# Performance work log

Hardware: AMD Instinct MI355X
Metric: run time of the kernel (lower is better)

## Reference

```python
import jax, jax.numpy as jnp
import numpy as np

H = 97
IN = 9
N_NODES = 100000
N_EDGES = 800000
N_GRAPHS = 4096
N_LAYERS = 7
N_STEPS = 7
BN_EPS = 1e-5


def setup_inputs() -> dict:
    key = jax.random.key(0)
    ks = iter(jax.random.split(key, 40))
    sc = 0.1  # param init scale
    inp = {}
    inp['x'] = jax.random.normal(next(ks), (N_NODES, IN), jnp.float32)
    inp['edge_index'] = jax.random.randint(next(ks), (2, N_EDGES), 0, N_NODES, jnp.int32)
    inp['batch'] = jnp.sort(jax.random.randint(next(ks), (N_NODES,), 0, N_GRAPHS, jnp.int32))
    inp['num_graphs'] = N_GRAPHS
    inp['lin1_W'] = jax.random.normal(next(ks), (IN, H), jnp.float32) * sc
    inp['lin1_b'] = jax.random.normal(next(ks), (H,), jnp.float32) * sc
    for nm in ['Wk', 'Wq', 'Wv', 'Ws']:
        inp['conv_' + nm] = jax.random.normal(next(ks), (N_LAYERS, H, H), jnp.float32) * sc
    for nm in ['bk', 'bq', 'bv', 'bs']:
        inp['conv_' + nm] = jax.random.normal(next(ks), (N_LAYERS, H), jnp.float32) * sc
    inp['gru_Wih'] = jax.random.normal(next(ks), (N_LAYERS, H, 3 * H), jnp.float32) * sc
    inp['gru_Whh'] = jax.random.normal(next(ks), (N_LAYERS, H, 3 * H), jnp.float32) * sc
    inp['gru_bih'] = jax.random.normal(next(ks), (N_LAYERS, 3 * H), jnp.float32) * sc
    inp['gru_bhh'] = jax.random.normal(next(ks), (N_LAYERS, 3 * H), jnp.float32) * sc
    inp['bn_gamma'] = jnp.ones((N_LAYERS - 1, H), jnp.float32)
    inp['bn_beta'] = jnp.zeros((N_LAYERS - 1, H), jnp.float32)
    inp['bn_mean'] = jnp.zeros((N_LAYERS - 1, H), jnp.float32)
    inp['bn_var'] = jnp.ones((N_LAYERS - 1, H), jnp.float32)
    inp['gat_W'] = jax.random.normal(next(ks), (H, H), jnp.float32) * sc
    inp['gat_asrc'] = jax.random.normal(next(ks), (H,), jnp.float32) * sc
    inp['gat_adst'] = jax.random.normal(next(ks), (H,), jnp.float32) * sc
    inp['gat_b'] = jax.random.normal(next(ks), (H,), jnp.float32) * sc
    inp['molgru_Wih'] = jax.random.normal(next(ks), (H, 3 * H), jnp.float32) * sc
    inp['molgru_Whh'] = jax.random.normal(next(ks), (H, 3 * H), jnp.float32) * sc
    inp['molgru_bih'] = jax.random.normal(next(ks), (3 * H,), jnp.float32) * sc
    inp['molgru_bhh'] = jax.random.normal(next(ks), (3 * H,), jnp.float32) * sc
    inp['lin2_W'] = jax.random.normal(next(ks), (H, 1), jnp.float32) * sc
    inp['lin2_b'] = jax.random.normal(next(ks), (1,), jnp.float32) * sc
    return inp


def _gru(xin, h, Wih, Whh, bih, bhh):
    gi = xin @ Wih + bih  # [N, 3H]
    gh = h @ Whh + bhh
    ir, iz, inn = jnp.split(gi, 3, axis=-1)
    hr, hz, hn = jnp.split(gh, 3, axis=-1)
    r = jax.nn.sigmoid(ir + hr)
    z = jax.nn.sigmoid(iz + hz)
    n = jnp.tanh(inn + r * hn)
    return (1.0 - z) * n + z * h


def _resgated(x, src, dst, Wk, bk, Wq, bq, Wv, bv, Ws, bs, n_nodes):
    # PyG ResGatedGraphConv: out_i = Ws x_i + sum_j sigmoid(Wk x_i + Wq x_j) * (Wv x_j)
    k = x @ Wk + bk
    q = x @ Wq + bq
    v = x @ Wv + bv
    msg = jax.nn.sigmoid(k[dst] + q[src]) * v[src]  # [E, H]
    agg = jax.ops.segment_sum(msg, dst, num_segments=n_nodes)
    return agg + (x @ Ws + bs)


def _forward(x, lin1_W, lin1_b, conv_Wk, conv_bk, conv_Wq, conv_bq, conv_Wv, conv_bv,
             conv_Ws, conv_bs, gru_Wih, gru_Whh, gru_bih, gru_bhh,
             bn_gamma, bn_beta, bn_mean, bn_var,
             gat_W, gat_asrc, gat_adst, gat_b,
             molgru_Wih, molgru_Whh, molgru_bih, molgru_bhh,
             lin2_W, lin2_b, edge_index, batch, num_graphs):
    src, dst = edge_index[0], edge_index[1]
    n_nodes = x.shape[0]
    x = jax.nn.leaky_relu(x @ lin1_W + lin1_b, 0.01)
    # layer 0 (gate_conv + gru)
    h = jax.nn.elu(_resgated(x, src, dst, conv_Wk[0], conv_bk[0], conv_Wq[0], conv_bq[0],
                             conv_Wv[0], conv_bv[0], conv_Ws[0], conv_bs[0], n_nodes))
    x = jax.nn.relu(_gru(h, x, gru_Wih[0], gru_Whh[0], gru_bih[0], gru_bhh[0]))
    # layers 1..6 with eval-mode BatchNorm (dropout inactive in eval)
    for l in range(1, N_LAYERS):
        h = jax.nn.elu(_resgated(x, src, dst, conv_Wk[l], conv_bk[l], conv_Wq[l], conv_bq[l],
                                 conv_Wv[l], conv_bv[l], conv_Ws[l], conv_bs[l], n_nodes))
        b = l - 1
        h = (h - bn_mean[b]) * (bn_gamma[b] / jnp.sqrt(bn_var[b] + BN_EPS)) + bn_beta[b]
        x = jax.nn.relu(_gru(h, x, gru_Wih[l], gru_Whh[l], gru_bih[l], gru_bhh[l]))
    # molecule readout: global_add_pool then bipartite GAT (heads=1) over node->graph edges
    out = jax.nn.relu(jax.ops.segment_sum(x, batch, num_segments=num_graphs))  # [G, H]
    xs = x @ gat_W          # source projections, fixed over timesteps
    a_s = xs @ gat_asrc     # [N]
    for _ in range(N_STEPS):
        a_d = (out @ gat_W) @ gat_adst  # [G]
        alpha = jax.nn.leaky_relu(a_s + a_d[batch], 0.01)  # one score per node-edge
        m = jax.ops.segment_max(alpha, batch, num_segments=num_graphs)
        m = jnp.where(jnp.isfinite(m), m, 0.0)
        e = jnp.exp(alpha - m[batch])
        s = jax.ops.segment_sum(e, batch, num_segments=num_graphs)
        w = e / s[batch]  # segment softmax over each graph's nodes
        hg = jax.ops.segment_sum(w[:, None] * xs, batch, num_segments=num_graphs) + gat_b
        h = jax.nn.elu(hg)
        out = jax.nn.relu(_gru(h, out, molgru_Wih, molgru_Whh, molgru_bih, molgru_bhh))
    return out @ lin2_W + lin2_b  # [G, 1]


def reference(x, edge_index, batch, num_graphs, lin1_W, lin1_b, conv_Wk, conv_bk, conv_Wq,
              conv_bq, conv_Wv, conv_bv, conv_Ws, conv_bs, gru_Wih, gru_Whh, gru_bih, gru_bhh,
              bn_gamma, bn_beta, bn_mean, bn_var, gat_W, gat_asrc, gat_adst, gat_b,
              molgru_Wih, molgru_Whh, molgru_bih, molgru_bhh, lin2_W, lin2_b):
    return _forward(x, lin1_W, lin1_b, conv_Wk, conv_bk, conv_Wq, conv_bq, conv_Wv, conv_bv,
                    conv_Ws, conv_bs, gru_Wih, gru_Whh, gru_bih, gru_bhh,
                    bn_gamma, bn_beta, bn_mean, bn_var,
                    gat_W, gat_asrc, gat_adst, gat_b,
                    molgru_Wih, molgru_Whh, molgru_bih, molgru_bhh,
                    lin2_W, lin2_b, edge_index, batch, num_graphs)
```

## Files before the change

kernel.cpp:

```cpp
#include <hip/hip_runtime.h>

#define NN 100000
#define NNP 100032
#define NE 800000
#define NG 4096
#define HH 97
#define HP 128
#define NB 391

#define WGF_SET_STRIDE 147456
#define WCF_LAYER_STRIDE 98304

typedef unsigned short u16;
typedef unsigned int u32;
typedef __attribute__((ext_vector_type(8))) short short8v;
typedef __attribute__((ext_vector_type(4))) float f32x4;

__device__ __forceinline__ float sigm_(float x){ return 1.f/(1.f+__expf(-x)); }
__device__ __forceinline__ float lrelu01_(float x){ return x>0.f? x : 0.01f*x; }
__device__ __forceinline__ float tanh_(float t){ float e2=__expf(2.f*t); return 1.f-2.f/(e2+1.f); }
__device__ __forceinline__ float b2f(u16 u){ union{u32 i; float f;} t; t.i=(u32)u<<16; return t.f; }
__device__ __forceinline__ u16 f2b(float x){ union{float f; u32 i;} t; t.f=x; u32 r=t.i+0x7FFFu+((t.i>>16)&1u); return (u16)(r>>16); }

__device__ __forceinline__ void store_bf16x4(u16* p, float v0, float v1, float v2, float v3){
  ushort4 s; s.x = f2b(v0); s.y = f2b(v1); s.z = f2b(v2); s.w = f2b(v3);
  *(ushort4*)p = s;
}

__device__ __forceinline__ f32x4 mfma16(short8v a, short8v b, f32x4 c){
  return __builtin_amdgcn_mfma_f32_16x16x32_bf16(a, b, c, 0, 0, 0);
}

__global__ void k_pack_convw(const float* __restrict__ Wk, const float* __restrict__ Wq,
                             const float* __restrict__ Wv, const float* __restrict__ Ws,
                             u16* __restrict__ out){
  int idx = blockIdx.x*256 + threadIdx.x;
  if (idx >= 7*4*8*3*2*512) return;
  int e = idx & 7, lane = (idx>>3) & 63;
  int r = idx >> 9;
  int term = r & 1; r >>= 1;
  int ks = r % 3; r /= 3;
  int t = r & 7; r >>= 3;
  int w = r & 3; int l = r >> 2;
  int k = ks*32 + (lane>>4)*8 + e;
  int n = (w*8 + t)*16 + (lane & 15);
  int m = n>>7, h = n & 127;
  float val = 0.f;
  if (k < HH && h < HH){
    const float* W = (m==0)? Wk : (m==1)? Wq : (m==2)? Wv : Ws;
    val = W[l*9409 + k*97 + h];
  }
  u16 hi = f2b(val);
  out[idx] = (term==0)? hi : f2b(val - b2f(hi));
}

__global__ void k_pack_gruw(const float* __restrict__ gih, const float* __restrict__ ghh,
                            const float* __restrict__ mih, const float* __restrict__ mhh,
                            u16* __restrict__ out){
  int idx = blockIdx.x*256 + threadIdx.x;
  if (idx >= 8*8*3*3*4*512) return;
  int e = idx & 7, lane = (idx>>3) & 63;
  int r = idx >> 9;
  int mat = r & 3; r >>= 2;
  int ks = r % 3; r /= 3;
  int j = r % 3; r /= 3;
  int bt = r & 7; int set = r >> 3;
  int k = ks*32 + (lane>>4)*8 + e;
  int n = (j*8 + bt)*16 + (lane & 15);
  int jg = n>>7, g = n & 127;
  float val = 0.f;
  if (k < HH && g < HH){
    const float* srcp;
    if (mat < 2) srcp = (set < 7)? gih + (size_t)set*28227 : mih;
    else         srcp = (set < 7)? ghh + (size_t)set*28227 : mhh;
    val = srcp[k*291 + jg*97 + g];
  }
  u16 hi = f2b(val);
  out[idx] = ((mat & 1)==0)? hi : f2b(val - b2f(hi));
}

__global__ void k_pack_gatw(const float* __restrict__ gatW, u16* __restrict__ out){
  int idx = blockIdx.x*256 + threadIdx.x;
  if (idx >= 2*4*8*512) return;
  int e = idx & 7, lane = (idx>>3) & 63, t = (idx>>9) & 7;
  int ks = (idx>>12) & 3, term = idx>>14;
  int k = ks*32 + (lane>>4)*8 + e;
  int h = t*16 + (lane & 15);
  float val = (k < HH && h < HH)? gatW[k*97 + h] : 0.f;
  u16 hi = f2b(val);
  out[idx] = (term==0)? hi : f2b(val - b2f(hi));
}

__global__ void k_pack_w96(const float* __restrict__ Wk, const float* __restrict__ Wq,
                           const float* __restrict__ Wv, const float* __restrict__ Ws,
                           const float* __restrict__ gih, const float* __restrict__ ghh,
                           const float* __restrict__ mih, const float* __restrict__ mhh,
                           float* __restrict__ out){
  int idx = blockIdx.x*256 + threadIdx.x;
  if (idx < 7*512){
    int l = idx >> 9, c = idx & 511;
    int m = c >> 7, h = c & 127;
    float v = 0.f;
    if (h < HH){
      const float* W = (m==0)? Wk : (m==1)? Wq : (m==2)? Wv : Ws;
      v = W[l*9409 + 96*97 + h];
    }
    out[idx] = v;
  } else if (idx < 7*512 + 8*384){
    int r = idx - 7*512;
    int set = r / 384, n = r % 384;
    int j = n >> 7, g = n & 127;
    float v = 0.f;
    if (g < HH){
      const float* srcp = (set < 7)? gih + (size_t)set*28227 : mih;
      v = srcp[96*291 + j*97 + g];
    }
    out[idx] = v;
  } else if (idx < 7*512 + 16*384){
    int r = idx - 7*512 - 8*384;
    int set = r / 384, n = r % 384;
    int j = n >> 7, g = n & 127;
    float v = 0.f;
    if (g < HH){
      const float* srcp = (set < 7)? ghh + (size_t)set*28227 : mhh;
      v = srcp[96*291 + j*97 + g];
    }
    out[idx] = v;
  }
}

__global__ void k_pack_convb(const float* __restrict__ bk, const float* __restrict__ bq,
                             const float* __restrict__ bv, const float* __restrict__ bs,
                             float* __restrict__ out){
  int idx = blockIdx.x*256 + threadIdx.x;
  if (idx >= 7*512) return;
  int l = idx >> 9, c = idx & 511;
  int m = c >> 7, h = c & 127;
  float v = 0.f;
  if (h < HH){
    const float* B = (m==0)? bk : (m==1)? bq : (m==2)? bv : bs;
    v = B[l*97 + h];
  }
  out[idx] = v;
}

__global__ void k_pack_grub(const float* __restrict__ gbi, const float* __restrict__ gbh,
                            const float* __restrict__ mbi, const float* __restrict__ mbh,
                            float* __restrict__ obi, float* __restrict__ obh){
  int idx = blockIdx.x*256 + threadIdx.x;
  if (idx >= 8*384) return;
  int set = idx / 384, n = idx % 384;
  int j = n>>7, g = n & 127;
  float vi = 0.f, vh = 0.f;
  if (g < HH){
    const float* si = (set < 7)? gbi + set*291 : mbi;
    const float* sh = (set < 7)? gbh + set*291 : mbh;
    vi = si[j*97 + g];
    vh = sh[j*97 + g];
  }
  obi[idx] = vi; obh[idx] = vh;
}

__global__ void k_pack_misc(const float* __restrict__ gatW, const float* __restrict__ asrc,
                            const float* __restrict__ adst, const float* __restrict__ gatb,
                            const float* __restrict__ l2W, float* __restrict__ out){
  int idx = blockIdx.x*256 + threadIdx.x;
  if (idx < 16384){
    int k = idx >> 7, h = idx & 127;
    out[idx] = (k < HH && h < HH)? gatW[k*97 + h] : 0.f;
  } else if (idx < 16512){
    int h = idx - 16384; out[idx] = (h < HH)? asrc[h] : 0.f;
  } else if (idx < 16640){
    int h = idx - 16512; out[idx] = (h < HH)? adst[h] : 0.f;
  } else if (idx < 16768){
    int h = idx - 16640; out[idx] = (h < HH)? gatb[h] : 0.f;
  } else if (idx < 16896){
    int h = idx - 16768; out[idx] = (h < HH)? l2W[h] : 0.f;
  } else if (idx < 17408){
    out[idx] = 0.f;
  }
}

__global__ void k_seg(const int* __restrict__ batch, int* __restrict__ seg){
  int g = blockIdx.x*blockDim.x + threadIdx.x;
  if (g > NG) return;
  int lo = 0, hi = NN;
  while (lo < hi){ int mid = (lo+hi) >> 1; if (batch[mid] < g) lo = mid+1; else hi = mid; }
  seg[g] = lo;
}

__global__ void k_hist(const int* __restrict__ dst, int* __restrict__ cnt){
  int e = blockIdx.x*256 + threadIdx.x;
  if (e < NE) atomicAdd(&cnt[dst[e]], 1);
}

__global__ void k_scan_blk(const int* __restrict__ cnt, int* __restrict__ offs,
                           int* __restrict__ bsum){
  __shared__ int s[256];
  int b = blockIdx.x, t = threadIdx.x, i = b*256 + t;
  int v = (i < NN)? cnt[i] : 0;
  s[t] = v; __syncthreads();
  #pragma unroll
  for (int off = 1; off < 256; off <<= 1){
    int tmp = (t >= off)? s[t-off] : 0;
    __syncthreads();
    s[t] += tmp;
    __syncthreads();
  }
  if (i < NN) offs[i] = s[t] - v;
  if (t == 255) bsum[b] = s[255];
}

__global__ void k_scan_top(int* __restrict__ bsum){
  __shared__ int s[512];
  int t = threadIdx.x;
  int v = (t < NB)? bsum[t] : 0;
  s[t] = v; __syncthreads();
  #pragma unroll
  for (int off = 1; off < 512; off <<= 1){
    int tmp = (t >= off)? s[t-off] : 0;
    __syncthreads();
    s[t] += tmp;
    __syncthreads();
  }
  if (t < NB) bsum[t] = s[t] - v;
}

__global__ void k_scan_add(int* __restrict__ offs, const int* __restrict__ bsum,
                           int* __restrict__ cur){
  int b = blockIdx.x, t = threadIdx.x, i = b*256 + t;
  if (i < NN){ int o = offs[i] + bsum[b]; offs[i] = o; cur[i] = o; }
  if (i == 0) offs[NN] = NE;
}

__global__ void k_scatter(const int* __restrict__ src, const int* __restrict__ dst,
                          int* __restrict__ cur, int* __restrict__ eidx){
  int e = blockIdx.x*256 + threadIdx.x;
  if (e >= NE) return;
  int pos = atomicAdd(&cur[dst[e]], 1);
  eidx[pos] = src[e];
}

__global__ __launch_bounds__(256) void k_lin1(const float* __restrict__ x,
    const float* __restrict__ W, const float* __restrict__ b, u16* __restrict__ X0){
  int idx = blockIdx.x*256 + threadIdx.x;
  int n = idx >> 7, c = idx & 127;
  float v = 0.f;
  if (n < NN && c < HH){
    v = b[c];
    #pragma unroll
    for (int k = 0; k < 9; ++k) v += x[n*9 + k]*W[k*HH + c];
    v = lrelu01_(v);
  }
  X0[(size_t)n*HP + c] = f2b(v);
}

__global__ __launch_bounds__(256) void k_conv_mfma(const u16* __restrict__ X,
    const u16* __restrict__ WCF_l, const float* __restrict__ biasp,
    const float* __restrict__ W96C, u16* __restrict__ KQV,
    u16* __restrict__ Sh, u16* __restrict__ Sl){
  int tid = threadIdx.x;
  int w = __builtin_amdgcn_readfirstlane(tid >> 6);
  int lane = tid & 63;
  int lm = lane & 15, ls = lane >> 4;
  int m0 = blockIdx.x*64;
  f32x4 acc[4][8] = {};
  const u16* pw = WCF_l + (size_t)w*24576 + lane*8;
  for (int ks = 0; ks < 3; ++ks){
    short8v aX[4];
    #pragma unroll
    for (int rb = 0; rb < 4; ++rb)
      aX[rb] = *(const short8v*)(X + (size_t)(m0 + rb*16 + lm)*HP + ks*32 + ls*8);
    short8v wf[8][2];
    #pragma unroll
    for (int t = 0; t < 8; ++t){
      const u16* q = pw + ((t*3 + ks) << 10);
      wf[t][0] = *(const short8v*)(q);
      wf[t][1] = *(const short8v*)(q + 512);
    }
    #pragma unroll
    for (int t = 0; t < 8; ++t)
      #pragma unroll
      for (int rb = 0; rb < 4; ++rb){
        acc[rb][t] = mfma16(wf[t][0], aX[rb], acc[rb][t]);
        acc[rb][t] = mfma16(wf[t][1], aX[rb], acc[rb][t]);
      }
  }
  float x96[4];
  #pragma unroll
  for (int rb = 0; rb < 4; ++rb)
    x96[rb] = b2f(X[(size_t)(m0 + rb*16 + lm)*HP + 96]);
  #pragma unroll
  for (int t = 0; t < 8; ++t){
    int c0 = w*128 + t*16 + ls*4;
    float4 bv = *(const float4*)(biasp + c0);
    float4 w96 = *(const float4*)(W96C + c0);
    #pragma unroll
    for (int rb = 0; rb < 4; ++rb){
      int node = m0 + rb*16 + lm;
      float v0 = acc[rb][t][0] + bv.x + x96[rb]*w96.x;
      float v1 = acc[rb][t][1] + bv.y + x96[rb]*w96.y;
      float v2 = acc[rb][t][2] + bv.z + x96[rb]*w96.z;
      float v3 = acc[rb][t][3] + bv.w + x96[rb]*w96.w;
      if (w < 3){
        store_bf16x4(KQV + (size_t)node*384 + w*128 + t*16 + ls*4, v0, v1, v2, v3);
      } else {
        int co = t*16 + ls*4;
        u16 h0 = f2b(v0), h1 = f2b(v1), h2 = f2b(v2), h3 = f2b(v3);
        ushort4 hv; hv.x=h0; hv.y=h1; hv.z=h2; hv.w=h3;
        *(ushort4*)(Sh + (size_t)node*HP + co) = hv;
        store_bf16x4(Sl + (size_t)node*HP + co,
                     v0 - b2f(h0), v1 - b2f(h1), v2 - b2f(h2), v3 - b2f(h3));
      }
    }
  }
}

__global__ __launch_bounds__(256) void k_gru_mfma(const u16* __restrict__ Sh_,
    const u16* __restrict__ Sl_, const u16* __restrict__ Xin,
    const u16* __restrict__ WGF_set,
    const float* __restrict__ bihp, const float* __restrict__ bhhp,
    const float* __restrict__ W96I, const float* __restrict__ W96H,
    u16* __restrict__ Xout){
  int tid = threadIdx.x;
  int w = __builtin_amdgcn_readfirstlane(tid >> 6);
  int lane = tid & 63;
  int lm = lane & 15, ls = lane >> 4;
  int m0 = blockIdx.x*32;
  f32x4 agi[2][2][3] = {};
  f32x4 agh[2][2][3] = {};
  for (int ks = 0; ks < 3; ++ks){
    short8v aX[2], aSh[2], aSl[2];
    #pragma unroll
    for (int rb = 0; rb < 2; ++rb){
      size_t off = (size_t)(m0 + rb*16 + lm)*HP + ks*32 + ls*8;
      aX[rb]  = *(const short8v*)(Xin + off);
      aSh[rb] = *(const short8v*)(Sh_ + off);
      aSl[rb] = *(const short8v*)(Sl_ + off);
    }
    #pragma unroll
    for (int b = 0; b < 2; ++b){
      const u16* pb = WGF_set + (size_t)(2*w + b)*18432 + lane*8;
      short8v fIh[3], fIl[3], fHh[3], fHl[3];
      #pragma unroll
      for (int j = 0; j < 3; ++j){
        const u16* q = pb + ((j*3 + ks) << 11);
        fIh[j] = *(const short8v*)(q);
        fIl[j] = *(const short8v*)(q + 512);
        fHh[j] = *(const short8v*)(q + 1024);
        fHl[j] = *(const short8v*)(q + 1536);
      }
      #pragma unroll
      for (int j = 0; j < 3; ++j)
        #pragma unroll
        for (int rb = 0; rb < 2; ++rb){
          agi[rb][b][j] = mfma16(fIh[j], aSh[rb], agi[rb][b][j]);
          agi[rb][b][j] = mfma16(fIl[j], aSh[rb], agi[rb][b][j]);
          agi[rb][b][j] = mfma16(fIh[j], aSl[rb], agi[rb][b][j]);
          agh[rb][b][j] = mfma16(fHh[j], aX[rb], agh[rb][b][j]);
          agh[rb][b][j] = mfma16(fHl[j], aX[rb], agh[rb][b][j]);
        }
    }
  }
  float s96[2], x96[2];
  #pragma unroll
  for (int rb = 0; rb < 2; ++rb){
    size_t o96 = (size_t)(m0 + rb*16 + lm)*HP + 96;
    s96[rb] = b2f(Sh_[o96]) + b2f(Sl_[o96]);
    x96[rb] = b2f(Xin[o96]);
  }
  #pragma unroll
  for (int b = 0; b < 2; ++b){
    int g0 = (2*w + b)*16 + ls*4;
    float4 bi0 = *(const float4*)(bihp + g0);
    float4 bi1 = *(const float4*)(bihp + 128 + g0);
    float4 bi2 = *(const float4*)(bihp + 256 + g0);
    float4 bh0 = *(const float4*)(bhhp + g0);
    float4 bh1 = *(const float4*)(bhhp + 128 + g0);
    float4 bh2 = *(const float4*)(bhhp + 256 + g0);
    float4 wi0 = *(const float4*)(W96I + g0);
    float4 wi1 = *(const float4*)(W96I + 128 + g0);
    float4 wi2 = *(const float4*)(W96I + 256 + g0);
    float4 wh0 = *(const float4*)(W96H + g0);
    float4 wh1 = *(const float4*)(W96H + 128 + g0);
    float4 wh2 = *(const float4*)(W96H + 256 + g0);
    #pragma unroll
    for (int rb = 0; rb < 2; ++rb){
      int node = m0 + rb*16 + lm;
      ushort4 xo4 = *(const ushort4*)(Xin + (size_t)node*HP + g0);
      float xo[4] = { b2f(xo4.x), b2f(xo4.y), b2f(xo4.z), b2f(xo4.w) };
      float vout[4];
      #pragma unroll
      for (int r = 0; r < 4; ++r){
        float biv0 = ((const float*)&bi0)[r], biv1 = ((const float*)&bi1)[r], biv2 = ((const float*)&bi2)[r];
        float bhv0 = ((const float*)&bh0)[r], bhv1 = ((const float*)&bh1)[r], bhv2 = ((const float*)&bh2)[r];
        float wiv0 = ((const float*)&wi0)[r], wiv1 = ((const float*)&wi1)[r], wiv2 = ((const float*)&wi2)[r];
        float whv0 = ((const float*)&wh0)[r], whv1 = ((const float*)&wh1)[r], whv2 = ((const float*)&wh2)[r];
        float ir = agi[rb][b][0][r] + biv0 + s96[rb]*wiv0;
        float iz = agi[rb][b][1][r] + biv1 + s96[rb]*wiv1;
        float in_ = agi[rb][b][2][r] + biv2 + s96[rb]*wiv2;
        float hr = agh[rb][b][0][r] + bhv0 + x96[rb]*whv0;
        float hz = agh[rb][b][1][r] + bhv1 + x96[rb]*whv1;
        float hn = agh[rb][b][2][r] + bhv2 + x96[rb]*whv2;
        float rr = sigm_(ir + hr);
        float zz = sigm_(iz + hz);
        float nn2 = tanh_(in_ + rr*hn);
        float v = (1.f - zz)*nn2 + zz*xo[r];
        vout[r] = fmaxf(v, 0.f);
      }
      store_bf16x4(Xout + (size_t)node*HP + g0, vout[0], vout[1], vout[2], vout[3]);
    }
  }
}

__global__ __launch_bounds__(256) void k_xs_mfma(const u16* __restrict__ X,
    const u16* __restrict__ GATF, u16* __restrict__ XS){
  int tid = threadIdx.x;
  int w = tid >> 6, lane = tid & 63;
  int lm = lane & 15, ls = lane >> 4;
  int m0 = blockIdx.x*32;
  f32x4 acc[2][2] = {};
  for (int ks = 0; ks < 4; ++ks){
    short8v aX[2];
    #pragma unroll
    for (int rb = 0; rb < 2; ++rb){
      int row = m0 + rb*16 + lm;
      aX[rb] = *(const short8v*)(X + (size_t)row*HP + ks*32 + ls*8);
    }
    #pragma unroll
    for (int b = 0; b < 2; ++b){
      int t = 2*w + b;
      short8v bh = *(const short8v*)(GATF + (((size_t)(0*4 + ks)*8 + t)*64 + lane)*8);
      short8v bl = *(const short8v*)(GATF + (((size_t)(1*4 + ks)*8 + t)*64 + lane)*8);
      #pragma unroll
      for (int rb = 0; rb < 2; ++rb){
        acc[rb][b] = mfma16(bh, aX[rb], acc[rb][b]);
        acc[rb][b] = mfma16(bl, aX[rb], acc[rb][b]);
      }
    }
  }
  #pragma unroll
  for (int b = 0; b < 2; ++b){
    int c0 = (2*w + b)*16 + ls*4;
    #pragma unroll
    for (int rb = 0; rb < 2; ++rb){
      int node = m0 + rb*16 + lm;
      store_bf16x4(XS + (size_t)node*HP + c0,
                   acc[rb][b][0], acc[rb][b][1], acc[rb][b][2], acc[rb][b][3]);
    }
  }
}

__global__ __launch_bounds__(256) void k_agg(const u16* __restrict__ kqv,
    const int* __restrict__ offs, const int* __restrict__ eidx,
    u16* __restrict__ Sh, u16* __restrict__ Sl,
    const float* __restrict__ gamma, const float* __restrict__ beta,
    const float* __restrict__ mean, const float* __restrict__ var, int layer){
  int n = blockIdx.x*4 + (threadIdx.x >> 6);
  if (n >= NN) return;
  int lane = threadIdx.x & 63;
  int c2 = lane*2;
  int lo = offs[n], hi = offs[n+1];
  ushort2 kk = *(const ushort2*)(kqv + (size_t)n*384 + c2);
  float k0 = b2f(kk.x), k1 = b2f(kk.y);
  float a0 = 0.f, a1 = 0.f;
  int i = lo;
  for (; i + 4 <= hi; i += 4){
    int s0 = eidx[i], s1 = eidx[i+1], s2 = eidx[i+2], s3 = eidx[i+3];
    const u16* q0 = kqv + (size_t)s0*384 + 128 + c2;
    const u16* q1 = kqv + (size_t)s1*384 + 128 + c2;
    const u16* q2 = kqv + (size_t)s2*384 + 128 + c2;
    const u16* q3 = kqv + (size_t)s3*384 + 128 + c2;
    ushort2 qa = *(const ushort2*)q0, va = *(const ushort2*)(q0 + 128);
    ushort2 qb = *(const ushort2*)q1, vb = *(const ushort2*)(q1 + 128);
    ushort2 qc = *(const ushort2*)q2, vc = *(const ushort2*)(q2 + 128);
    ushort2 qd = *(const ushort2*)q3, vd = *(const ushort2*)(q3 + 128);
    a0 += b2f(va.x)*sigm_(k0 + b2f(qa.x)); a1 += b2f(va.y)*sigm_(k1 + b2f(qa.y));
    a0 += b2f(vb.x)*sigm_(k0 + b2f(qb.x)); a1 += b2f(vb.y)*sigm_(k1 + b2f(qb.y));
    a0 += b2f(vc.x)*sigm_(k0 + b2f(qc.x)); a1 += b2f(vc.y)*sigm_(k1 + b2f(qc.y));
    a0 += b2f(vd.x)*sigm_(k0 + b2f(qd.x)); a1 += b2f(vd.y)*sigm_(k1 + b2f(qd.y));
  }
  for (; i < hi; ++i){
    int s = eidx[i];
    const u16* qb0 = kqv + (size_t)s*384 + 128 + c2;
    ushort2 qq = *(const ushort2*)qb0;
    ushort2 vv = *(const ushort2*)(qb0 + 128);
    a0 += b2f(vv.x)*sigm_(k0 + b2f(qq.x));
    a1 += b2f(vv.y)*sigm_(k1 + b2f(qq.y));
  }
  u16* shp = Sh + (size_t)n*HP + c2;
  u16* slp = Sl + (size_t)n*HP + c2;
  ushort2 sh2 = *(const ushort2*)shp;
  ushort2 sl2 = *(const ushort2*)slp;
  float v0 = b2f(sh2.x) + b2f(sl2.x) + a0;
  float v1 = b2f(sh2.y) + b2f(sl2.y) + a1;
  v0 = v0 > 0.f ? v0 : (__expf(v0) - 1.f);
  v1 = v1 > 0.f ? v1 : (__expf(v1) - 1.f);
  if (layer > 0){
    int b0 = (layer-1)*97 + c2;
    if (c2 < HH){ float sc = gamma[b0]*rsqrtf(var[b0] + 1e-5f); v0 = (v0 - mean[b0])*sc + beta[b0]; }
    if (c2+1 < HH){ float sc = gamma[b0+1]*rsqrtf(var[b0+1] + 1e-5f); v1 = (v1 - mean[b0+1])*sc + beta[b0+1]; }
  }
  if (c2 >= HH)   v0 = 0.f;
  if (c2+1 >= HH) v1 = 0.f;
  u16 h0 = f2b(v0), h1 = f2b(v1);
  *(ushort2*)shp = make_ushort2(h0, h1);
  *(ushort2*)slp = make_ushort2(f2b(v0 - b2f(h0)), f2b(v1 - b2f(h1)));
}

__global__ __launch_bounds__(128) void k_pool(const int* __restrict__ seg,
    const u16* __restrict__ x, u16* __restrict__ out){
  int g = blockIdx.x, tid = threadIdx.x;
  int lo = seg[g], hi = seg[g+1];
  float acc = 0.f;
  for (int n = lo; n < hi; ++n) acc += b2f(x[(size_t)n*HP + tid]);
  out[(size_t)g*HP + tid] = f2b(fmaxf(acc, 0.f));
}

__global__ __launch_bounds__(256) void k_as(const u16* __restrict__ xs,
    const float* __restrict__ asrcp, float* __restrict__ a_s){
  int t = blockIdx.x*256 + threadIdx.x;
  int n = t >> 6, lane = t & 63;
  float v = b2f(xs[(size_t)n*HP + lane])*asrcp[lane]
          + b2f(xs[(size_t)n*HP + 64 + lane])*asrcp[64 + lane];
  #pragma unroll
  for (int o = 32; o > 0; o >>= 1) v += __shfl_down(v, o);
  if (lane == 0) a_s[n] = v;
}

__global__ __launch_bounds__(128) void k_ad(const u16* __restrict__ out,
    const float* __restrict__ gatwp, const float* __restrict__ adstp, float* __restrict__ ad){
  int g = blockIdx.x, tid = threadIdx.x;
  __shared__ float so[HP];
  __shared__ float red[2];
  so[tid] = b2f(out[(size_t)g*HP + tid]);
  __syncthreads();
  float p = 0.f;
  #pragma unroll 4
  for (int k = 0; k < HP; ++k) p += so[k]*gatwp[k*HP + tid];
  float v = p * adstp[tid];
  #pragma unroll
  for (int o = 32; o > 0; o >>= 1) v += __shfl_down(v, o);
  if ((tid & 63) == 0) red[tid >> 6] = v;
  __syncthreads();
  if (tid == 0) ad[g] = red[0] + red[1];
}

#define ACAP 2048
__global__ __launch_bounds__(128) void k_attn(const int* __restrict__ seg,
    const float* __restrict__ a_s, const float* __restrict__ a_d,
    const u16* __restrict__ xs, const float* __restrict__ gbp,
    u16* __restrict__ hgh, u16* __restrict__ hgl){
  int g = blockIdx.x, tid = threadIdx.x;
  int lo = seg[g], hi = seg[g+1], cnt = hi - lo;
  float ad = a_d[g];
  __shared__ float sa[ACAP];
  __shared__ float red[2];
  float mloc = -3.4e38f;
  for (int i = tid; i < cnt; i += 128){
    float al = lrelu01_(a_s[lo+i] + ad);
    if (i < ACAP) sa[i] = al;
    mloc = fmaxf(mloc, al);
  }
  #pragma unroll
  for (int o = 32; o > 0; o >>= 1) mloc = fmaxf(mloc, __shfl_down(mloc, o));
  if ((tid & 63) == 0) red[tid >> 6] = mloc;
  __syncthreads();
  float mm = fmaxf(red[0], red[1]);
  __syncthreads();
  float sloc = 0.f;
  for (int i = tid; i < cnt; i += 128){
    float al = (i < ACAP)? sa[i] : lrelu01_(a_s[lo+i] + ad);
    float e = __expf(al - mm);
    if (i < ACAP) sa[i] = e;
    sloc += e;
  }
  #pragma unroll
  for (int o = 32; o > 0; o >>= 1) sloc += __shfl_down(sloc, o);
  if ((tid & 63) == 0) red[tid >> 6] = sloc;
  __syncthreads();
  float ss = red[0] + red[1];
  float inv = (cnt > 0 && ss != 0.f)? 1.f/ss : 0.f;
  __syncthreads();
  float accv = 0.f;
  for (int i = 0; i < cnt; ++i){
    float e = (i < ACAP)? sa[i] : __expf(lrelu01_(a_s[lo+i] + ad) - mm);
    accv += (e*inv) * b2f(xs[(size_t)(lo+i)*HP + tid]);
  }
  float hgv = accv + gbp[tid];
  hgv = hgv > 0.f ? hgv : (__expf(hgv) - 1.f);
  u16 hb = f2b(hgv);
  hgh[(size_t)g*HP + tid] = hb;
  hgl[(size_t)g*HP + tid] = f2b(hgv - b2f(hb));
}

__global__ __launch_bounds__(64) void k_final(const u16* __restrict__ out,
    const float* __restrict__ w2p, const float* __restrict__ l2b, float* __restrict__ y){
  int g = blockIdx.x, lane = threadIdx.x;
  float v = b2f(out[(size_t)g*HP + lane])*w2p[lane]
          + b2f(out[(size_t)g*HP + 64 + lane])*w2p[64 + lane];
  #pragma unroll
  for (int o = 32; o > 0; o >>= 1) v += __shfl_down(v, o);
  if (lane == 0) y[g] = v + l2b[0];
}

extern "C" void kernel_launch(void* const* d_in, const int* in_sizes, int n_in,
                              void* d_out, int out_size, void* d_ws, size_t ws_size,
                              hipStream_t stream){
  const float* x_in  = (const float*)d_in[0];
  const int*   ei    = (const int*)d_in[1];
  const int*   batch = (const int*)d_in[2];
  const float* lin1W = (const float*)d_in[4];
  const float* lin1b = (const float*)d_in[5];
  const float* cWk = (const float*)d_in[6];
  const float* cWq = (const float*)d_in[7];
  const float* cWv = (const float*)d_in[8];
  const float* cWs = (const float*)d_in[9];
  const float* cbk = (const float*)d_in[10];
  const float* cbq = (const float*)d_in[11];
  const float* cbv = (const float*)d_in[12];
  const float* cbs = (const float*)d_in[13];
  const float* gWih = (const float*)d_in[14];
  const float* gWhh = (const float*)d_in[15];
  const float* gbih = (const float*)d_in[16];
  const float* gbhh = (const float*)d_in[17];
  const float* bng = (const float*)d_in[18];
  const float* bnb = (const float*)d_in[19];
  const float* bnm = (const float*)d_in[20];
  const float* bnv = (const float*)d_in[21];
  const float* gatW  = (const float*)d_in[22];
  const float* gasrc = (const float*)d_in[23];
  const float* gadst = (const float*)d_in[24];
  const float* gatb  = (const float*)d_in[25];
  const float* mWih = (const float*)d_in[26];
  const float* mWhh = (const float*)d_in[27];
  const float* mbih = (const float*)d_in[28];
  const float* mbhh = (const float*)d_in[29];
  const float* l2W = (const float*)d_in[30];
  const float* l2b = (const float*)d_in[31];
  const int* src = ei;
  const int* dst = ei + NE;

  char* base = (char*)d_ws;
  size_t off = 0;
  auto alloc = [&](size_t nbytes)->char*{
    char* p = base + off; off = (off + nbytes + 255) & ~(size_t)255; return p; };

  u16*  WCF  = (u16*)alloc((size_t)7*WCF_LAYER_STRIDE*2);
  u16*  WGF  = (u16*)alloc((size_t)8*WGF_SET_STRIDE*2);
  u16*  GATF = (u16*)alloc((size_t)2*4*8*512*2);
  float* W96  = (float*)alloc((size_t)(7*512 + 16*384)*4);
  float* BCONVP = (float*)alloc(7*512*4);
  float* BIHP   = (float*)alloc(8*384*4);
  float* BHHP   = (float*)alloc(8*384*4);
  float* GATWP  = (float*)alloc(17408*4);
  float* ASRCP = GATWP + 16384;
  float* ADSTP = GATWP + 16512;
  float* GBP   = GATWP + 16640;
  float* W2P   = GATWP + 16768;
  u16*  X0  = (u16*)alloc((size_t)NNP*HP*2);
  u16*  X1  = (u16*)alloc((size_t)NNP*HP*2);
  u16*  KQV = (u16*)alloc((size_t)NNP*384*2);
  u16*  Sh  = (u16*)alloc((size_t)NNP*HP*2);
  u16*  Sl  = (u16*)alloc((size_t)NNP*HP*2);
  float* AS_ = (float*)alloc((size_t)NN*4);
  float* AD_ = (float*)alloc((size_t)NG*4);
  u16*  OUTA = (u16*)alloc((size_t)NG*HP*2);
  u16*  OUTB = (u16*)alloc((size_t)NG*HP*2);
  u16*  HGH  = (u16*)alloc((size_t)NG*HP*2);
  u16*  HGL  = (u16*)alloc((size_t)NG*HP*2);
  int*  SEG  = (int*)alloc((size_t)(NG+1)*4);
  int*  CNT  = (int*)alloc((size_t)NN*4);
  int*  OFFS = (int*)alloc((size_t)(NN+1)*4);
  int*  CUR  = (int*)alloc((size_t)NN*4);
  int*  EIDX = (int*)alloc((size_t)NE*4);
  int*  BSUM = (int*)alloc((size_t)NB*4);

  float* W96C = W96;
  float* W96I = W96 + 7*512;
  float* W96H = W96 + 7*512 + 8*384;

  if (ws_size < off){
    hipMemsetAsync(d_out, 0, (size_t)out_size*sizeof(float), stream);
    return;
  }

  k_pack_convw<<<(7*WCF_LAYER_STRIDE)/256,256,0,stream>>>(cWk,cWq,cWv,cWs,WCF);
  k_pack_gruw<<<(8*WGF_SET_STRIDE)/256,256,0,stream>>>(gWih,gWhh,mWih,mWhh,WGF);
  k_pack_gatw<<<(2*4*8*512+255)/256,256,0,stream>>>(gatW,GATF);
  k_pack_w96<<<(7*512+16*384+255)/256,256,0,stream>>>(cWk,cWq,cWv,cWs,gWih,gWhh,mWih,mWhh,W96);
  k_pack_convb<<<(7*512+255)/256,256,0,stream>>>(cbk,cbq,cbv,cbs,BCONVP);
  k_pack_grub<<<(8*384+255)/256,256,0,stream>>>(gbih,gbhh,mbih,mbhh,BIHP,BHHP);
  k_pack_misc<<<68,256,0,stream>>>(gatW,gasrc,gadst,gatb,l2W,GATWP);
  k_lin1<<<(NNP*HP)/256,256,0,stream>>>(x_in,lin1W,lin1b,X0);
  k_seg<<<(NG+1+255)/256,256,0,stream>>>(batch,SEG);

  hipMemsetAsync(CNT, 0, (size_t)NN*4, stream);
  k_hist<<<(NE+255)/256,256,0,stream>>>(dst, CNT);
  k_scan_blk<<<NB,256,0,stream>>>(CNT, OFFS, BSUM);
  k_scan_top<<<1,512,0,stream>>>(BSUM);
  k_scan_add<<<NB,256,0,stream>>>(OFFS, BSUM, CUR);
  k_scatter<<<(NE+255)/256,256,0,stream>>>(src, dst, CUR, EIDX);

  for (int l = 0; l < 7; ++l){
    u16* Xin  = (l & 1)? X1 : X0;
    u16* Xout = (l & 1)? X0 : X1;
    k_conv_mfma<<<NNP/64,256,0,stream>>>(Xin, WCF + (size_t)l*WCF_LAYER_STRIDE,
                                         BCONVP + l*512, W96C + l*512, KQV, Sh, Sl);
    k_agg<<<(NN+3)/4,256,0,stream>>>(KQV, OFFS, EIDX, Sh, Sl, bng, bnb, bnm, bnv, l);
    k_gru_mfma<<<NNP/32,256,0,stream>>>(Sh, Sl, Xin, WGF + (size_t)l*WGF_SET_STRIDE,
                                        BIHP + l*384, BHHP + l*384,
                                        W96I + l*384, W96H + l*384, Xout);
  }
  u16* XF = X1;

  k_pool<<<NG,128,0,stream>>>(SEG, XF, OUTA);
  u16* XS = KQV;
  k_xs_mfma<<<NNP/32,256,0,stream>>>(XF, GATF, XS);
  k_as<<<(NN*64)/256,256,0,stream>>>(XS, ASRCP, AS_);

  u16* cur = OUTA; u16* nxt = OUTB;
  for (int s = 0; s < 7; ++s){
    k_ad<<<NG,128,0,stream>>>(cur, GATWP, ADSTP, AD_);
    k_attn<<<NG,128,0,stream>>>(SEG, AS_, AD_, XS, GBP, HGH, HGL);
    k_gru_mfma<<<NG/32,256,0,stream>>>(HGH, HGL, cur, WGF + (size_t)7*WGF_SET_STRIDE,
                                       BIHP + 7*384, BHHP + 7*384,
                                       W96I + 7*384, W96H + 7*384, nxt);
    u16* t = cur; cur = nxt; nxt = t;
  }
  k_final<<<NG,64,0,stream>>>(cur, W2P, l2b, (float*)d_out);
}
```

Before: 2.722 ms.

## Stage MFMA epilogue outputs through shared memory for coalesced 16-byte stores

The conv, GRU and XS MFMA kernels now write their bf16 results into a padded LDS tile and then copy them out with row-contiguous 16-byte global stores, replacing the scattered 8-byte per-lane stores. The conv kernel also halves its node tile from 64 to 32 rows per block and doubles the grid, so it keeps fewer accumulators per thread. The change adds LDS use and a block barrier per kernel, and each block now reuses the conv weight fragments over half as many rows.

```diff
diff --git a/kernel.cpp b/kernel.cpp
--- a/kernel.cpp
+++ b/kernel.cpp
@@ -10,6 +10,7 @@
 
 #define WGF_SET_STRIDE 147456
 #define WCF_LAYER_STRIDE 98304
+#define LSTR 136
 
 typedef unsigned short u16;
 typedef unsigned int u32;
@@ -22,7 +23,7 @@
 __device__ __forceinline__ float b2f(u16 u){ union{u32 i; float f;} t; t.i=(u32)u<<16; return t.f; }
 __device__ __forceinline__ u16 f2b(float x){ union{float f; u32 i;} t; t.f=x; u32 r=t.i+0x7FFFu+((t.i>>16)&1u); return (u16)(r>>16); }
 
-__device__ __forceinline__ void store_bf16x4(u16* p, float v0, float v1, float v2, float v3){
+__device__ __forceinline__ void stg_bf16x4(u16* p, float v0, float v1, float v2, float v3){
   ushort4 s; s.x = f2b(v0); s.y = f2b(v1); s.z = f2b(v2); s.w = f2b(v3);
   *(ushort4*)p = s;
 }
@@ -259,17 +260,18 @@
     const u16* __restrict__ WCF_l, const float* __restrict__ biasp,
     const float* __restrict__ W96C, u16* __restrict__ KQV,
     u16* __restrict__ Sh, u16* __restrict__ Sl){
+  __shared__ u16 stg[5][32][LSTR];
   int tid = threadIdx.x;
   int w = __builtin_amdgcn_readfirstlane(tid >> 6);
   int lane = tid & 63;
   int lm = lane & 15, ls = lane >> 4;
-  int m0 = blockIdx.x*64;
-  f32x4 acc[4][8] = {};
+  int m0 = blockIdx.x*32;
+  f32x4 acc[2][8] = {};
   const u16* pw = WCF_l + (size_t)w*24576 + lane*8;
   for (int ks = 0; ks < 3; ++ks){
-    short8v aX[4];
-    #pragma unroll
-    for (int rb = 0; rb < 4; ++rb)
+    short8v aX[2];
+    #pragma unroll
+    for (int rb = 0; rb < 2; ++rb)
       aX[rb] = *(const short8v*)(X + (size_t)(m0 + rb*16 + lm)*HP + ks*32 + ls*8);
     short8v wf[8][2];
     #pragma unroll
@@ -281,14 +283,14 @@
     #pragma unroll
     for (int t = 0; t < 8; ++t)
       #pragma unroll
-      for (int rb = 0; rb < 4; ++rb){
+      for (int rb = 0; rb < 2; ++rb){
         acc[rb][t] = mfma16(wf[t][0], aX[rb], acc[rb][t]);
         acc[rb][t] = mfma16(wf[t][1], aX[rb], acc[rb][t]);
       }
   }
-  float x96[4];
-  #pragma unroll
-  for (int rb = 0; rb < 4; ++rb)
+  float x96[2];
+  #pragma unroll
+  for (int rb = 0; rb < 2; ++rb)
     x96[rb] = b2f(X[(size_t)(m0 + rb*16 + lm)*HP + 96]);
   #pragma unroll
   for (int t = 0; t < 8; ++t){
@@ -296,22 +298,40 @@
     float4 bv = *(const float4*)(biasp + c0);
     float4 w96 = *(const float4*)(W96C + c0);
     #pragma unroll
-    for (int rb = 0; rb < 4; ++rb){
-      int node = m0 + rb*16 + lm;
+    for (int rb = 0; rb < 2; ++rb){
+      int node = rb*16 + lm;
+      int co = t*16 + ls*4;
       float v0 = acc[rb][t][0] + bv.x + x96[rb]*w96.x;
       float v1 = acc[rb][t][1] + bv.y + x96[rb]*w96.y;
       float v2 = acc[rb][t][2] + bv.z + x96[rb]*w96.z;
       float v3 = acc[rb][t][3] + bv.w + x96[rb]*w96.w;
       if (w < 3){
-        store_bf16x4(KQV + (size_t)node*384 + w*128 + t*16 + ls*4, v0, v1, v2, v3);
+        stg_bf16x4(&stg[w][node][co], v0, v1, v2, v3);
       } else {
-        int co = t*16 + ls*4;
         u16 h0 = f2b(v0), h1 = f2b(v1), h2 = f2b(v2), h3 = f2b(v3);
         ushort4 hv; hv.x=h0; hv.y=h1; hv.z=h2; hv.w=h3;
-        *(ushort4*)(Sh + (size_t)node*HP + co) = hv;
-        store_bf16x4(Sl + (size_t)node*HP + co,
-                     v0 - b2f(h0), v1 - b2f(h1), v2 - b2f(h2), v3 - b2f(h3));
+        *(ushort4*)&stg[3][node][co] = hv;
+        stg_bf16x4(&stg[4][node][co],
+                   v0 - b2f(h0), v1 - b2f(h1), v2 - b2f(h2), v3 - b2f(h3));
       }
+    }
+  }
+  __syncthreads();
+  if (w < 3){
+    #pragma unroll
+    for (int it = 0; it < 8; ++it){
+      int q = it*64 + lane;
+      int node = q >> 4, ch = q & 15;
+      *(short8v*)(KQV + (size_t)(m0 + node)*384 + w*128 + ch*8) =
+          *(const short8v*)&stg[w][node][ch*8];
+    }
+  } else {
+    #pragma unroll
+    for (int it = 0; it < 8; ++it){
+      int q = it*64 + lane;
+      int node = q >> 4, ch = q & 15;
+      *(short8v*)(Sh + (size_t)m0*128 + q*8) = *(const short8v*)&stg[3][node][ch*8];
+      *(short8v*)(Sl + (size_t)m0*128 + q*8) = *(const short8v*)&stg[4][node][ch*8];
     }
   }
 }
@@ -322,6 +342,7 @@
     const float* __restrict__ bihp, const float* __restrict__ bhhp,
     const float* __restrict__ W96I, const float* __restrict__ W96H,
     u16* __restrict__ Xout){
+  __shared__ u16 stg[32][LSTR];
   int tid = threadIdx.x;
   int w = __builtin_amdgcn_readfirstlane(tid >> 6);
   int lane = tid & 63;
@@ -386,8 +407,8 @@
     float4 wh2 = *(const float4*)(W96H + 256 + g0);
     #pragma unroll
     for (int rb = 0; rb < 2; ++rb){
-      int node = m0 + rb*16 + lm;
-      ushort4 xo4 = *(const ushort4*)(Xin + (size_t)node*HP + g0);
+      int node = rb*16 + lm;
+      ushort4 xo4 = *(const ushort4*)(Xin + (size_t)(m0 + node)*HP + g0);
       float xo[4] = { b2f(xo4.x), b2f(xo4.y), b2f(xo4.z), b2f(xo4.w) };
       float vout[4];
       #pragma unroll
@@ -408,15 +429,24 @@
         float v = (1.f - zz)*nn2 + zz*xo[r];
         vout[r] = fmaxf(v, 0.f);
       }
-      store_bf16x4(Xout + (size_t)node*HP + g0, vout[0], vout[1], vout[2], vout[3]);
-    }
+      stg_bf16x4(&stg[node][g0], vout[0], vout[1], vout[2], vout[3]);
+    }
+  }
+  __syncthreads();
+  #pragma unroll
+  for (int it = 0; it < 2; ++it){
+    int q = it*256 + tid;
+    int node = q >> 4, ch = q & 15;
+    *(short8v*)(Xout + (size_t)m0*128 + q*8) = *(const short8v*)&stg[node][ch*8];
   }
 }
 
 __global__ __launch_bounds__(256) void k_xs_mfma(const u16* __restrict__ X,
     const u16* __restrict__ GATF, u16* __restrict__ XS){
+  __shared__ u16 stg[32][LSTR];
   int tid = threadIdx.x;
-  int w = tid >> 6, lane = tid & 63;
+  int w = __builtin_amdgcn_readfirstlane(tid >> 6);
+  int lane = tid & 63;
   int lm = lane & 15, ls = lane >> 4;
   int m0 = blockIdx.x*32;
   f32x4 acc[2][2] = {};
@@ -444,10 +474,16 @@
     int c0 = (2*w + b)*16 + ls*4;
     #pragma unroll
     for (int rb = 0; rb < 2; ++rb){
-      int node = m0 + rb*16 + lm;
-      store_bf16x4(XS + (size_t)node*HP + c0,
-                   acc[rb][b][0], acc[rb][b][1], acc[rb][b][2], acc[rb][b][3]);
-    }
+      int node = rb*16 + lm;
+      stg_bf16x4(&stg[node][c0], acc[rb][b][0], acc[rb][b][1], acc[rb][b][2], acc[rb][b][3]);
+    }
+  }
+  __syncthreads();
+  #pragma unroll
+  for (int it = 0; it < 2; ++it){
+    int q = it*256 + tid;
+    int node = q >> 4, ch = q & 15;
+    *(short8v*)(XS + (size_t)m0*128 + q*8) = *(const short8v*)&stg[node][ch*8];
   }
 }
 
@@ -705,7 +741,7 @@
   for (int l = 0; l < 7; ++l){
     u16* Xin  = (l & 1)? X1 : X0;
     u16* Xout = (l & 1)? X0 : X1;
-    k_conv_mfma<<<NNP/64,256,0,stream>>>(Xin, WCF + (size_t)l*WCF_LAYER_STRIDE,
+    k_conv_mfma<<<NNP/32,256,0,stream>>>(Xin, WCF + (size_t)l*WCF_LAYER_STRIDE,
                                          BCONVP + l*512, W96C + l*512, KQV, Sh, Sl);
     k_agg<<<(NN+3)/4,256,0,stream>>>(KQV, OFFS, EIDX, Sh, Sl, bng, bnb, bnm, bnv, l);
     k_gru_mfma<<<NNP/32,256,0,stream>>>(Sh, Sl, Xin, WGF + (size_t)l*WGF_SET_STRIDE,
```

After: 2.270 ms. -16.6%, faster.
